# Optimization experiments

Hardware: AMD Instinct MI355X
Metric: run time of the kernel (lower is better)

Reference implementation:

```python
import jax, jax.numpy as jnp
import numpy as np

BS, N, HD, NW = 4, 512, 64, 2
IN_DIM = 2 * HD * NW  # 256, fc1 input
EMB = HD              # node embedding dim (fc2 output)

# static off-diagonal indices (mask = ~eye)
_rows, _cols = np.nonzero(~np.eye(N, dtype=bool))
ROWS = jnp.asarray(_rows)
COLS = jnp.asarray(_cols)


def _leaky(x):
    return jnp.where(x > 0, x, 0.01 * x)


def setup_inputs() -> dict:
    key = jax.random.key(0)
    ks = jax.random.split(key, 10)
    s = lambda fan_in: 1.0 / np.sqrt(fan_in)
    return {
        "node_features": jax.random.normal(ks[0], (BS, N, IN_DIM), jnp.float32),
        "fc1_w": jax.random.normal(ks[1], (IN_DIM, 2 * HD), jnp.float32) * s(IN_DIM),
        "fc1_b": jnp.zeros((2 * HD,), jnp.float32),
        "fc2_w": jax.random.normal(ks[2], (2 * HD, EMB), jnp.float32) * s(2 * HD),
        "fc2_b": jnp.zeros((EMB,), jnp.float32),
        "e1_w": jax.random.normal(ks[3], (2 * EMB, EMB), jnp.float32) * s(2 * EMB),
        "e1_b": jnp.zeros((EMB,), jnp.float32),
        "e2_w": jax.random.normal(ks[4], (EMB, 2), jnp.float32) * s(EMB),
        "e2_b": jnp.zeros((2,), jnp.float32),
    }


def reference(node_features, fc1_w, fc1_b, fc2_w, fc2_b, e1_w, e1_b, e2_w, e2_b):
    # fc head (dropout = identity at inference)
    h = _leaky(jnp.einsum('bnf,fh->bnh', node_features, fc1_w) + fc1_b)
    emb = _leaky(jnp.einsum('bnh,hd->bnd', h, fc2_w) + fc2_b)  # [bs, N, EMB]

    # O(N^2) pairwise broadcast: hi - hj and hi * hj, concat -> edge MLP
    hi = emb[:, :, None, :]                 # [bs, N, 1, EMB]
    hj = emb[:, None, :, :]                 # [bs, 1, N, EMB]
    edge_in = jnp.concatenate([hi - hj, hi * hj], axis=-1)  # [bs, N, N, 2*EMB]

    eh = jnp.maximum(jnp.einsum('bijf,fh->bijh', edge_in, e1_w) + e1_b, 0.0)
    logits = jnp.einsum('bijh,hk->bijk', eh, e2_w) + e2_b    # [bs, N, N, 2]
    edge_prob = jax.nn.softmax(logits, axis=-1)

    adjacency_matrix = edge_prob[..., 1]                     # [bs, N, N]
    # masked gather of off-diagonal entries, both class probs, flattened per batch
    prediction = edge_prob[:, ROWS, COLS, :].reshape(edge_prob.shape[0], -1)
    return adjacency_matrix, prediction, emb
```

## Files before the change

kernel.cpp:

```cpp
#include <hip/hip_runtime.h>
#include <hip/hip_bf16.h>

#define BSZ 4
#define NN 512
#define INDIM 256
#define H1 128
#define EMBD 64

#define PRED_OFF  (BSZ*NN*NN)
#define PRED_PER_B (NN*(NN-1)*2)
#define EMB_OFF   (PRED_OFF + BSZ*PRED_PER_B)

typedef __attribute__((ext_vector_type(8))) short bf16x8;
typedef __attribute__((ext_vector_type(4))) float f32x4;

__device__ __forceinline__ short bfs(float x) {
  return (short)__builtin_bit_cast(unsigned short, __float2bfloat16(x));
}
__device__ __forceinline__ bf16x8 pack8(float4 a, float4 b) {
  bf16x8 r;
  r[0] = bfs(a.x); r[1] = bfs(a.y); r[2] = bfs(a.z); r[3] = bfs(a.w);
  r[4] = bfs(b.x); r[5] = bfs(b.y); r[6] = bfs(b.z); r[7] = bfs(b.w);
  return r;
}

__global__ __launch_bounds__(256) void k1_embed(
    const float* __restrict__ nf, const float* __restrict__ fc1w,
    const float* __restrict__ fc1b, const float* __restrict__ fc2w,
    const float* __restrict__ fc2b, float* __restrict__ out)
{
  __shared__ float nfs[4][INDIM];
  __shared__ float hs[4][H1];
  const int t = threadIdx.x;
  const int nb = blockIdx.x * 4;

  {
    const int nd = t >> 6, off = (t & 63) * 4;
    *reinterpret_cast<float4*>(&nfs[nd][off]) =
        *reinterpret_cast<const float4*>(nf + (size_t)(nb + nd) * INDIM + off);
  }
  __syncthreads();
  {
    const int c = t & 127, grp = t >> 7;
    float a0 = 0.f, a1 = 0.f;
    for (int f = 0; f < INDIM; ++f) {
      const float w = fc1w[f * H1 + c];
      a0 = fmaf(nfs[grp][f], w, a0);
      a1 = fmaf(nfs[grp + 2][f], w, a1);
    }
    const float bb = fc1b[c];
    a0 += bb; a1 += bb;
    hs[grp][c]     = a0 > 0.f ? a0 : 0.01f * a0;
    hs[grp + 2][c] = a1 > 0.f ? a1 : 0.01f * a1;
  }
  __syncthreads();
  {
    const int d = t & 63, nd = t >> 6;
    float acc = 0.f;
    for (int f = 0; f < H1; ++f) acc = fmaf(hs[nd][f], fc2w[f * EMBD + d], acc);
    acc += fc2b[d];
    const float e = acc > 0.f ? acc : 0.01f * acc;
    out[EMB_OFF + (size_t)(nb + nd) * EMBD + d] = e;
  }
}

__global__ __launch_bounds__(256) void k2_edges(
    const float* __restrict__ e1w, const float* __restrict__ e1b,
    const float* __restrict__ e2w, const float* __restrict__ e2b,
    float* __restrict__ out)
{
  __shared__ __align__(16) __hip_bfloat16 Bm[64 * 72];
  __shared__ float embi[64];
  __shared__ float ash[64];
  const int t = threadIdx.x;
  const int b = blockIdx.x >> 9, i = blockIdx.x & 511;
  const float* __restrict__ Ef = out + EMB_OFF;

  if (t < 64) embi[t] = Ef[(size_t)(b * NN + i) * EMBD + t];
  __syncthreads();

  for (int idx = t; idx < 64 * 64; idx += 256) {
    const int dd = idx >> 6, hh = idx & 63;
    const float v = embi[dd] * e1w[(64 + dd) * 64 + hh] - e1w[dd * 64 + hh];
    Bm[hh * 72 + dd] = __float2bfloat16(v);
  }
  if (t < 64) {
    float acc = 0.f;
    for (int dd = 0; dd < 64; ++dd)
      acc = fmaf(embi[dd], e1w[dd * 64 + t], acc);
    ash[t] = acc + e1b[t];
  }
  __syncthreads();

  const int l = t & 63, wv = t >> 6;
  const int lg = l >> 4;
  const int ll = l & 15;

  float ci[16], wd[16];
#pragma unroll
  for (int mt = 0; mt < 4; ++mt)
#pragma unroll
    for (int r = 0; r < 4; ++r) {
      const int h = mt * 16 + lg * 4 + r;
      ci[mt * 4 + r] = ash[h];
      wd[mt * 4 + r] = e2w[2 * h + 1] - e2w[2 * h];
    }
  const float ldbias = e2b[1] - e2b[0];

  bf16x8 afr[4][2];
#pragma unroll
  for (int mt = 0; mt < 4; ++mt)
#pragma unroll
    for (int ks = 0; ks < 2; ++ks)
      afr[mt][ks] = *reinterpret_cast<const bf16x8*>(
          &Bm[(mt * 16 + ll) * 72 + ks * 32 + lg * 8]);

  const size_t adj_base = (size_t)(b * NN + i) * NN;
  const size_t pred_base = (size_t)PRED_OFF + (size_t)b * PRED_PER_B;

  for (int nt = 0; nt < 8; ++nt) {
    const int j0 = wv * 128 + nt * 16;
    const float* ef = Ef + ((size_t)(b * NN) + j0 + ll) * EMBD + lg * 8;
    const float4 fa = *reinterpret_cast<const float4*>(ef);
    const float4 fb = *reinterpret_cast<const float4*>(ef + 4);
    const float4 fc = *reinterpret_cast<const float4*>(ef + 32);
    const float4 fd = *reinterpret_cast<const float4*>(ef + 36);
    const bf16x8 b0 = pack8(fa, fb);
    const bf16x8 b1 = pack8(fc, fd);

    f32x4 acc[4] = {{0.f,0.f,0.f,0.f},{0.f,0.f,0.f,0.f},
                    {0.f,0.f,0.f,0.f},{0.f,0.f,0.f,0.f}};
#pragma unroll
    for (int mt = 0; mt < 4; ++mt) {
      acc[mt] = __builtin_amdgcn_mfma_f32_16x16x32_bf16(afr[mt][0], b0, acc[mt], 0, 0, 0);
      acc[mt] = __builtin_amdgcn_mfma_f32_16x16x32_bf16(afr[mt][1], b1, acc[mt], 0, 0, 0);
    }

    float ldp = 0.f;
#pragma unroll
    for (int mt = 0; mt < 4; ++mt)
#pragma unroll
      for (int r = 0; r < 4; ++r) {
        float eh = acc[mt][r] + ci[mt * 4 + r];
        eh = eh > 0.f ? eh : 0.f;
        ldp = fmaf(eh, wd[mt * 4 + r], ldp);
      }
    ldp += __shfl_xor(ldp, 16, 64);
    ldp += __shfl_xor(ldp, 32, 64);

    const float x = ldp + ldbias;
    const float tt = __expf(-fabsf(x));
    const float rr = 1.f / (1.f + tt);
    const float p1 = x >= 0.f ? rr : tt * rr;
    const float p0 = x >= 0.f ? tt * rr : rr;

    if (l < 16) {
      const int j = j0 + ll;
      out[adj_base + j] = p1;
      if (j != i) {
        const int jj = j - (j > i ? 1 : 0);
        *reinterpret_cast<float2*>(
            out + pred_base + ((size_t)i * (NN - 1) + jj) * 2) =
            make_float2(p0, p1);
      }
    }
  }
}

extern "C" void kernel_launch(void* const* d_in, const int* in_sizes, int n_in,
                              void* d_out, int out_size, void* d_ws, size_t ws_size,
                              hipStream_t stream) {
  const float* nf   = (const float*)d_in[0];
  const float* fc1w = (const float*)d_in[1];
  const float* fc1b = (const float*)d_in[2];
  const float* fc2w = (const float*)d_in[3];
  const float* fc2b = (const float*)d_in[4];
  const float* e1w  = (const float*)d_in[5];
  const float* e1b  = (const float*)d_in[6];
  const float* e2w  = (const float*)d_in[7];
  const float* e2b  = (const float*)d_in[8];
  float* out = (float*)d_out;

  k1_embed<<<BSZ * NN / 4, 256, 0, stream>>>(nf, fc1w, fc1b, fc2w, fc2b, out);
  k2_edges<<<BSZ * NN, 256, 0, stream>>>(e1w, e1b, e2w, e2b, out);
}
```

Before: 124.2 us.

## Process four rows per block, prefetch bf16 embeddings from workspace

Restructures the edge kernel so each block handles four query rows i, with each wave owning one row and sweeping all 512 columns, instead of four waves splitting a single row. When a workspace is available, the embed kernel also writes a bf16 copy of the embeddings, so the edge kernel loads packed bf16 operands directly instead of converting fp32. The next column tile is software-prefetched while MFMAs run on the current one. Block count drops fourfold and LDS usage grows fourfold, which may lower occupancy and parallelism.

```diff
diff --git a/kernel.cpp b/kernel.cpp
--- a/kernel.cpp
+++ b/kernel.cpp
@@ -12,22 +12,25 @@
 #define EMB_OFF   (PRED_OFF + BSZ*PRED_PER_B)
 
 typedef __attribute__((ext_vector_type(8))) short bf16x8;
+typedef __attribute__((ext_vector_type(4))) short bf16x4;
 typedef __attribute__((ext_vector_type(4))) float f32x4;
 
-__device__ __forceinline__ short bfs(float x) {
+static __device__ __forceinline__ short bfs(float x) {
   return (short)__builtin_bit_cast(unsigned short, __float2bfloat16(x));
 }
-__device__ __forceinline__ bf16x8 pack8(float4 a, float4 b) {
+static __device__ __forceinline__ bf16x8 pack8(float4 a, float4 b) {
   bf16x8 r;
   r[0] = bfs(a.x); r[1] = bfs(a.y); r[2] = bfs(a.z); r[3] = bfs(a.w);
   r[4] = bfs(b.x); r[5] = bfs(b.y); r[6] = bfs(b.z); r[7] = bfs(b.w);
   return r;
 }
 
+template<bool WS>
 __global__ __launch_bounds__(256) void k1_embed(
     const float* __restrict__ nf, const float* __restrict__ fc1w,
     const float* __restrict__ fc1b, const float* __restrict__ fc2w,
-    const float* __restrict__ fc2b, float* __restrict__ out)
+    const float* __restrict__ fc2b, float* __restrict__ out,
+    unsigned short* __restrict__ ebf)
 {
   __shared__ float nfs[4][INDIM];
   __shared__ float hs[4][H1];
@@ -60,39 +63,57 @@
     for (int f = 0; f < H1; ++f) acc = fmaf(hs[nd][f], fc2w[f * EMBD + d], acc);
     acc += fc2b[d];
     const float e = acc > 0.f ? acc : 0.01f * acc;
-    out[EMB_OFF + (size_t)(nb + nd) * EMBD + d] = e;
-  }
-}
-
+    const size_t idx = (size_t)(nb + nd) * EMBD + d;
+    out[EMB_OFF + idx] = e;
+    if (WS) ebf[idx] = (unsigned short)bfs(e);
+  }
+}
+
+template<bool WS>
 __global__ __launch_bounds__(256) void k2_edges(
     const float* __restrict__ e1w, const float* __restrict__ e1b,
     const float* __restrict__ e2w, const float* __restrict__ e2b,
-    float* __restrict__ out)
+    float* __restrict__ out, const unsigned short* __restrict__ ebf)
 {
-  __shared__ __align__(16) __hip_bfloat16 Bm[64 * 72];
-  __shared__ float embi[64];
-  __shared__ float ash[64];
+  __shared__ __align__(16) __hip_bfloat16 Bm[4][64 * 72];
+  __shared__ float embi[4][64];
+  __shared__ float ash[4][64];
   const int t = threadIdx.x;
-  const int b = blockIdx.x >> 9, i = blockIdx.x & 511;
+  const int b = blockIdx.x >> 7;
+  const int ibase = (blockIdx.x & 127) * 4;
   const float* __restrict__ Ef = out + EMB_OFF;
 
-  if (t < 64) embi[t] = Ef[(size_t)(b * NN + i) * EMBD + t];
-  __syncthreads();
-
-  for (int idx = t; idx < 64 * 64; idx += 256) {
-    const int dd = idx >> 6, hh = idx & 63;
-    const float v = embi[dd] * e1w[(64 + dd) * 64 + hh] - e1w[dd * 64 + hh];
-    Bm[hh * 72 + dd] = __float2bfloat16(v);
-  }
-  if (t < 64) {
+  {
+    const int ii = t >> 6, l0 = t & 63;
+    embi[ii][l0] = Ef[((size_t)(b * NN) + ibase + ii) * EMBD + l0];
+  }
+  __syncthreads();
+
+  {
+    const int hh = t & 63, sub = t >> 6;
+    for (int k = 0; k < 16; ++k) {
+      const int ii = k >> 2;
+      const int dd0 = (k & 3) * 16 + sub * 4;
+      bf16x4 w;
+#pragma unroll
+      for (int q = 0; q < 4; ++q) {
+        const int dd = dd0 + q;
+        const float v = embi[ii][dd] * e1w[(64 + dd) * 64 + hh] - e1w[dd * 64 + hh];
+        w[q] = bfs(v);
+      }
+      *reinterpret_cast<bf16x4*>(&Bm[ii][hh * 72 + dd0]) = w;
+    }
+  }
+
+  const int l = t & 63, wv = t >> 6;
+  {
     float acc = 0.f;
-    for (int dd = 0; dd < 64; ++dd)
-      acc = fmaf(embi[dd], e1w[dd * 64 + t], acc);
-    ash[t] = acc + e1b[t];
-  }
-  __syncthreads();
-
-  const int l = t & 63, wv = t >> 6;
+    for (int dd = 0; dd < EMBD; ++dd)
+      acc = fmaf(embi[wv][dd], e1w[dd * 64 + l], acc);
+    ash[wv][l] = acc + e1b[l];
+  }
+  __syncthreads();
+
   const int lg = l >> 4;
   const int ll = l & 15;
 
@@ -102,7 +123,7 @@
 #pragma unroll
     for (int r = 0; r < 4; ++r) {
       const int h = mt * 16 + lg * 4 + r;
-      ci[mt * 4 + r] = ash[h];
+      ci[mt * 4 + r] = ash[wv][h];
       wd[mt * 4 + r] = e2w[2 * h + 1] - e2w[2 * h];
     }
   const float ldbias = e2b[1] - e2b[0];
@@ -113,20 +134,36 @@
 #pragma unroll
     for (int ks = 0; ks < 2; ++ks)
       afr[mt][ks] = *reinterpret_cast<const bf16x8*>(
-          &Bm[(mt * 16 + ll) * 72 + ks * 32 + lg * 8]);
-
-  const size_t adj_base = (size_t)(b * NN + i) * NN;
-  const size_t pred_base = (size_t)PRED_OFF + (size_t)b * PRED_PER_B;
-
-  for (int nt = 0; nt < 8; ++nt) {
-    const int j0 = wv * 128 + nt * 16;
-    const float* ef = Ef + ((size_t)(b * NN) + j0 + ll) * EMBD + lg * 8;
-    const float4 fa = *reinterpret_cast<const float4*>(ef);
-    const float4 fb = *reinterpret_cast<const float4*>(ef + 4);
-    const float4 fc = *reinterpret_cast<const float4*>(ef + 32);
-    const float4 fd = *reinterpret_cast<const float4*>(ef + 36);
-    const bf16x8 b0 = pack8(fa, fb);
-    const bf16x8 b1 = pack8(fc, fd);
+          &Bm[wv][(mt * 16 + ll) * 72 + ks * 32 + lg * 8]);
+
+  const int i = ibase + wv;
+  const size_t adj_base = ((size_t)(b * NN) + i) * NN;
+  const size_t pred_base =
+      (size_t)PRED_OFF + (size_t)b * PRED_PER_B + (size_t)i * (NN - 1) * 2;
+
+  auto loadB = [&](int j0, bf16x8& o0, bf16x8& o1) {
+    if (WS) {
+      const unsigned short* p =
+          ebf + ((size_t)(b * NN) + j0 + ll) * EMBD + lg * 8;
+      o0 = *reinterpret_cast<const bf16x8*>(p);
+      o1 = *reinterpret_cast<const bf16x8*>(p + 32);
+    } else {
+      const float* ef = Ef + ((size_t)(b * NN) + j0 + ll) * EMBD + lg * 8;
+      const float4 fa = *reinterpret_cast<const float4*>(ef);
+      const float4 fb = *reinterpret_cast<const float4*>(ef + 4);
+      const float4 fc = *reinterpret_cast<const float4*>(ef + 32);
+      const float4 fd = *reinterpret_cast<const float4*>(ef + 36);
+      o0 = pack8(fa, fb);
+      o1 = pack8(fc, fd);
+    }
+  };
+
+  bf16x8 pb0, pb1;
+  loadB(0, pb0, pb1);
+
+  for (int nt = 0; nt < 32; ++nt) {
+    const bf16x8 b0 = pb0, b1 = pb1;
+    if (nt < 31) loadB((nt + 1) * 16, pb0, pb1);
 
     f32x4 acc[4] = {{0.f,0.f,0.f,0.f},{0.f,0.f,0.f,0.f},
                     {0.f,0.f,0.f,0.f},{0.f,0.f,0.f,0.f}};
@@ -155,12 +192,11 @@
     const float p0 = x >= 0.f ? tt * rr : rr;
 
     if (l < 16) {
-      const int j = j0 + ll;
+      const int j = nt * 16 + ll;
       out[adj_base + j] = p1;
       if (j != i) {
         const int jj = j - (j > i ? 1 : 0);
-        *reinterpret_cast<float2*>(
-            out + pred_base + ((size_t)i * (NN - 1) + jj) * 2) =
+        *reinterpret_cast<float2*>(out + pred_base + (size_t)jj * 2) =
             make_float2(p0, p1);
       }
     }
@@ -180,7 +216,14 @@
   const float* e2w  = (const float*)d_in[7];
   const float* e2b  = (const float*)d_in[8];
   float* out = (float*)d_out;
-
-  k1_embed<<<BSZ * NN / 4, 256, 0, stream>>>(nf, fc1w, fc1b, fc2w, fc2b, out);
-  k2_edges<<<BSZ * NN, 256, 0, stream>>>(e1w, e1b, e2w, e2b, out);
-}
+  unsigned short* ebf = (unsigned short*)d_ws;
+  const bool use_ws = ws_size >= (size_t)BSZ * NN * EMBD * sizeof(unsigned short);
+
+  if (use_ws) {
+    k1_embed<true><<<BSZ * NN / 4, 256, 0, stream>>>(nf, fc1w, fc1b, fc2w, fc2b, out, ebf);
+    k2_edges<true><<<BSZ * NN / 4, 256, 0, stream>>>(e1w, e1b, e2w, e2b, out, ebf);
+  } else {
+    k1_embed<false><<<BSZ * NN / 4, 256, 0, stream>>>(nf, fc1w, fc1b, fc2w, fc2b, out, nullptr);
+    k2_edges<false><<<BSZ * NN / 4, 256, 0, stream>>>(e1w, e1b, e2w, e2b, out, nullptr);
+  }
+}
```

Result: faster. 119.3 us (-3.9%).
